# Optimization experiments

Hardware: AMD Instinct MI355X
Metric: run time of the kernel (lower is better)

The kernel has to match this reference:

```python
import jax, jax.numpy as jnp
import numpy as np

N_CLASSES = 10
NBD_PAD = 1
EPS = 1e-5  # nn.LayerNorm default eps


def _neighbor_states(state, n):
    # state: [B, n_classes, H, W]; replicates F.unfold(kernel=2n+1, padding=n)
    # then drops the center tap. Kernel positions enumerated row-major, matching
    # unfold's (C, K2) channel ordering after the view in the torch code.
    B, C, H, W = state.shape
    k = 2 * n + 1
    center = (k * k) // 2
    padded = jnp.pad(state, ((0, 0), (0, 0), (n, n), (n, n)))
    shifts = []
    for idx in range(k * k):
        if idx == center:
            continue
        ki, kj = divmod(idx, k)
        shifts.append(padded[:, :, ki:ki + H, kj:kj + W])
    nb = jnp.stack(shifts, axis=2)  # [B, C, K2-1, H, W]
    return nb.reshape(B, C * (k * k - 1), H, W)


def setup_inputs() -> dict:
    key = jax.random.key(0)
    ks = jax.random.split(key, 7)
    B, C, H, W = 64, 32, 128, 128
    NN_HID, PERC = 128, 112
    x = jax.random.normal(ks[0], (B, C, H, W), dtype=jnp.float32)
    w1 = jax.random.normal(ks[1], (NN_HID, PERC), dtype=jnp.float32) * (1.0 / np.sqrt(PERC))
    b1 = jax.random.normal(ks[2], (NN_HID,), dtype=jnp.float32) * 0.02
    w2 = jax.random.normal(ks[3], (C, NN_HID), dtype=jnp.float32) * (1.0 / np.sqrt(NN_HID))
    b2 = jax.random.normal(ks[4], (C,), dtype=jnp.float32) * 0.02
    gamma = jnp.ones((C,), dtype=jnp.float32) + 0.1 * jax.random.normal(ks[5], (C,), dtype=jnp.float32)
    beta = 0.1 * jax.random.normal(ks[6], (C,), dtype=jnp.float32)
    return {"x": x, "w1": w1, "b1": b1, "w2": w2, "b2": b2, "gamma": gamma, "beta": beta}


def reference(x, w1, b1, w2, b2, gamma, beta):
    # perceive: [B, in_ch + n_classes*(K2-1), H, W]
    nb = _neighbor_states(x[:, :N_CLASSES], NBD_PAD)
    perc = jnp.concatenate([x, nb], axis=1)
    # 1x1 conv MLP (fire_rate == 1.0 -> no update mask)
    h = jax.nn.relu(jnp.einsum('bchw,oc->bohw', perc, w1) + b1[None, :, None, None])
    dx = jnp.einsum('bchw,oc->bohw', h, w2) + b2[None, :, None, None]
    new_state = x + dx
    # clean_slate_if_white: zero hidden channels where argmax class == 0 (no_grad mask)
    pred = jnp.argmax(new_state[:, :N_CLASSES], axis=1)  # [B,H,W]
    inv = jax.lax.stop_gradient((pred != 0).astype(new_state.dtype))[:, None]  # [B,1,H,W]
    new_state = jnp.concatenate(
        [new_state[:, :N_CLASSES], new_state[:, N_CLASSES:] * inv], axis=1)
    # LayerNorm over channel dim (torch permutes to NHWC, norms last dim, permutes back)
    mu = jnp.mean(new_state, axis=1, keepdims=True)
    var = jnp.var(new_state, axis=1, keepdims=True)
    xn = (new_state - mu) * jax.lax.rsqrt(var + EPS)
    return xn * gamma[None, :, None, None] + beta[None, :, None, None]
```

## Files before the change

kernel.cpp:

```cpp
#include <hip/hip_runtime.h>

typedef unsigned short U16;
typedef unsigned int U32;
typedef __bf16 bf16;
typedef bf16 bf16x8 __attribute__((ext_vector_type(8)));
typedef U16  u16x8  __attribute__((ext_vector_type(8)));
typedef float f32x4 __attribute__((ext_vector_type(4)));

__device__ __forceinline__ void split3(float a, U16& o1, U16& o2, U16& o3) {
    U32 ua = __float_as_uint(a);
    float a1 = __uint_as_float(ua & 0xFFFF0000u);
    float r1 = a - a1;
    U32 u2 = __float_as_uint(r1);
    float a2 = __uint_as_float(u2 & 0xFFFF0000u);
    float r2 = r1 - a2;
    o1 = (U16)(ua >> 16);
    o2 = (U16)(u2 >> 16);
    o3 = (U16)(__float_as_uint(r2) >> 16);
}

__device__ __forceinline__ void split3x8(const float v[8], bf16x8& A1, bf16x8& A2, bf16x8& A3) {
    u16x8 e1, e2, e3;
    #pragma unroll
    for (int j = 0; j < 8; ++j) { U16 a, b, c; split3(v[j], a, b, c); e1[j] = a; e2[j] = b; e3[j] = c; }
    A1 = __builtin_bit_cast(bf16x8, e1);
    A2 = __builtin_bit_cast(bf16x8, e2);
    A3 = __builtin_bit_cast(bf16x8, e3);
}

__global__ __launch_bounds__(256)
void prep_kernel(const float* __restrict__ w1g, const float* __restrict__ w2g,
                 U16* __restrict__ w1L, U16* __restrict__ w2L)
{
    int tid = blockIdx.x * 256 + threadIdx.x;
    if (tid < 2048) {
        int n = tid >> 4, k0 = (tid & 15) << 3;
        float v[8];
        #pragma unroll
        for (int j = 0; j < 8; ++j) { int k = k0 + j; v[j] = (k < 112) ? w1g[n * 112 + k] : 0.0f; }
        bf16x8 L1, L2, L3; split3x8(v, L1, L2, L3);
        *(bf16x8*)(w1L + 0 * 16384 + n * 128 + k0) = L1;
        *(bf16x8*)(w1L + 1 * 16384 + n * 128 + k0) = L2;
        *(bf16x8*)(w1L + 2 * 16384 + n * 128 + k0) = L3;
    }
    if (tid < 512) {
        int n = tid >> 4, k0 = (tid & 15) << 3;
        float v[8];
        #pragma unroll
        for (int j = 0; j < 8; ++j) v[j] = w2g[n * 128 + k0 + j];
        bf16x8 L1, L2, L3; split3x8(v, L1, L2, L3);
        *(bf16x8*)(w2L + 0 * 4096 + n * 128 + k0) = L1;
        *(bf16x8*)(w2L + 1 * 4096 + n * 128 + k0) = L2;
        *(bf16x8*)(w2L + 2 * 4096 + n * 128 + k0) = L3;
    }
}

__global__ __launch_bounds__(256, 3)
void cann_kernel(const float* __restrict__ xg,  const U16* __restrict__ w1L,
                 const U16* __restrict__ w2L,
                 const float* __restrict__ b1g, const float* __restrict__ b2g,
                 const float* __restrict__ gg,  const float* __restrict__ bg,
                 float* __restrict__ outg)
{
    __shared__ __align__(16) U16 sL[3 * 8704];

    const int tid  = threadIdx.x;
    const int bid  = blockIdx.x;
    const int jseg = bid & 1;
    const int irow = (bid >> 1) & 127;
    const int b    = bid >> 8;
    const int jbase = jseg << 6;
    const int lane = tid & 63;
    const int wv   = tid >> 6;
    const int quad = lane >> 4;
    const int col  = lane & 15;

    {
        int px = tid & 63;
        int cg = tid >> 6;
        const float* src = xg + (b * 32 + cg * 8) * 16384 + irow * 128 + jbase + px;
        float v[8];
        #pragma unroll
        for (int i = 0; i < 8; ++i) v[i] = src[i * 16384];
        bf16x8 L1, L2, L3; split3x8(v, L1, L2, L3);
        int o = px * 136 + cg * 8;
        *(bf16x8*)&sL[o] = L1;
        *(bf16x8*)&sL[8704 + o] = L2;
        *(bf16x8*)&sL[17408 + o] = L3;

        #pragma unroll
        for (int pass = 0; pass < 3; ++pass) {
            int j = tid + pass * 256;
            if (j < 640) {
                int tpx = j & 63, cls = j >> 6;
                const float* cbase = xg + (b * 32 + cls) * 16384;
                float tv[8];
                #pragma unroll
                for (int t = 0; t < 8; ++t) {
                    int di = (int)((0x22211000u >> (4 * t)) & 0xFu) - 1;
                    int dj = (int)((0x21020210u >> (4 * t)) & 0xFu) - 1;
                    int row = irow + di;
                    int cc  = jbase + tpx + dj;
                    tv[t] = ((unsigned)row < 128u && (unsigned)cc < 128u)
                            ? cbase[row * 128 + cc] : 0.0f;
                }
                bf16x8 T1, T2, T3; split3x8(tv, T1, T2, T3);
                int to = tpx * 136 + 32 + cls * 8;
                *(bf16x8*)&sL[to] = T1;
                *(bf16x8*)&sL[8704 + to] = T2;
                *(bf16x8*)&sL[17408 + to] = T3;
            }
        }
        if (tid < 128) {
            int zo = (tid >> 1) * 136 + 112 + (tid & 1) * 8;
            uint4 z = make_uint4(0u, 0u, 0u, 0u);
            *(uint4*)&sL[zo] = z;
            *(uint4*)&sL[8704 + zo] = z;
            *(uint4*)&sL[17408 + zo] = z;
        }
    }

    bf16x8 bw1[3][2][4];
    #pragma unroll
    for (int n2 = 0; n2 < 2; ++n2)
        #pragma unroll
        for (int ks = 0; ks < 4; ++ks) {
            int n  = wv * 32 + n2 * 16 + col;
            int k0 = ks * 32 + quad * 8;
            #pragma unroll
            for (int L = 0; L < 3; ++L)
                bw1[L][n2][ks] = *(const bf16x8*)(w1L + L * 16384 + n * 128 + k0);
        }
    const float b1v0 = b1g[wv * 32 + col];
    const float b1v1 = b1g[wv * 32 + 16 + col];
    const float b2v0 = b2g[col];
    const float b2v1 = b2g[16 + col];

    float xs[2][4];
    #pragma unroll
    for (int n2 = 0; n2 < 2; ++n2)
        #pragma unroll
        for (int r = 0; r < 4; ++r)
            xs[n2][r] = xg[(b * 32 + n2 * 16 + col) * 16384 + irow * 128 + jbase
                           + wv * 16 + quad * 4 + r];

    __syncthreads();

    const f32x4 fz = {0.f, 0.f, 0.f, 0.f};
    f32x4 acc1[4][2];
    #pragma unroll
    for (int mt = 0; mt < 4; ++mt) { acc1[mt][0] = fz; acc1[mt][1] = fz; }

    #pragma unroll
    for (int mt = 0; mt < 4; ++mt) {
        #pragma unroll
        for (int ks = 0; ks < 4; ++ks) {
            int ao = (mt * 16 + col) * 136 + ks * 32 + quad * 8;
            bf16x8 A1 = *(const bf16x8*)&sL[ao];
            bf16x8 A2 = *(const bf16x8*)&sL[8704 + ao];
            bf16x8 A3 = *(const bf16x8*)&sL[17408 + ao];
            #pragma unroll
            for (int n2 = 0; n2 < 2; ++n2) {
                f32x4 a = acc1[mt][n2];
                a = __builtin_amdgcn_mfma_f32_16x16x32_bf16(A1, bw1[0][n2][ks], a, 0, 0, 0);
                a = __builtin_amdgcn_mfma_f32_16x16x32_bf16(A1, bw1[1][n2][ks], a, 0, 0, 0);
                a = __builtin_amdgcn_mfma_f32_16x16x32_bf16(A2, bw1[0][n2][ks], a, 0, 0, 0);
                a = __builtin_amdgcn_mfma_f32_16x16x32_bf16(A1, bw1[2][n2][ks], a, 0, 0, 0);
                a = __builtin_amdgcn_mfma_f32_16x16x32_bf16(A2, bw1[1][n2][ks], a, 0, 0, 0);
                a = __builtin_amdgcn_mfma_f32_16x16x32_bf16(A3, bw1[0][n2][ks], a, 0, 0, 0);
                acc1[mt][n2] = a;
            }
        }
    }
    __syncthreads();

    #pragma unroll
    for (int mt = 0; mt < 4; ++mt)
        #pragma unroll
        for (int n2 = 0; n2 < 2; ++n2) {
            float bb = n2 ? b1v1 : b1v0;
            #pragma unroll
            for (int r = 0; r < 4; ++r) {
                float v = fmaxf(acc1[mt][n2][r] + bb, 0.0f);
                U16 u1, u2, u3; split3(v, u1, u2, u3);
                int ho = (mt * 16 + quad * 4 + r) * 136 + wv * 32 + n2 * 16 + col;
                sL[ho] = u1; sL[8704 + ho] = u2; sL[17408 + ho] = u3;
            }
        }
    __syncthreads();

    f32x4 acc2[2];
    acc2[0] = fz; acc2[1] = fz;
    #pragma unroll
    for (int ks = 0; ks < 4; ++ks) {
        int k0 = ks * 32 + quad * 8;
        int ho = (wv * 16 + col) * 136 + k0;
        bf16x8 H1 = *(const bf16x8*)&sL[ho];
        bf16x8 H2 = *(const bf16x8*)&sL[8704 + ho];
        bf16x8 H3 = *(const bf16x8*)&sL[17408 + ho];
        #pragma unroll
        for (int n2 = 0; n2 < 2; ++n2) {
            int bo = (n2 * 16 + col) * 128 + k0;
            bf16x8 B1 = *(const bf16x8*)(w2L + 0 * 4096 + bo);
            bf16x8 B2 = *(const bf16x8*)(w2L + 1 * 4096 + bo);
            bf16x8 B3 = *(const bf16x8*)(w2L + 2 * 4096 + bo);
            f32x4 a = acc2[n2];
            a = __builtin_amdgcn_mfma_f32_16x16x32_bf16(H1, B1, a, 0, 0, 0);
            a = __builtin_amdgcn_mfma_f32_16x16x32_bf16(H1, B2, a, 0, 0, 0);
            a = __builtin_amdgcn_mfma_f32_16x16x32_bf16(H2, B1, a, 0, 0, 0);
            a = __builtin_amdgcn_mfma_f32_16x16x32_bf16(H1, B3, a, 0, 0, 0);
            a = __builtin_amdgcn_mfma_f32_16x16x32_bf16(H2, B2, a, 0, 0, 0);
            a = __builtin_amdgcn_mfma_f32_16x16x32_bf16(H3, B1, a, 0, 0, 0);
            acc2[n2] = a;
        }
    }
    __syncthreads();

    float* dxl = (float*)sL;
    #pragma unroll
    for (int n2 = 0; n2 < 2; ++n2) {
        float bb = n2 ? b2v1 : b2v0;
        int c = n2 * 16 + col;
        #pragma unroll
        for (int r = 0; r < 4; ++r) {
            int p = wv * 16 + quad * 4 + r;
            dxl[p * 33 + c] = acc2[n2][r] + bb + xs[n2][r];
        }
    }
    __syncthreads();

    if (tid < 64) {
        int p = tid;
        float ns[32];
        #pragma unroll
        for (int c = 0; c < 32; ++c) ns[c] = dxl[p * 33 + c];
        float m = ns[1];
        #pragma unroll
        for (int c = 2; c < 10; ++c) m = fmaxf(m, ns[c]);
        float keep = (m > ns[0]) ? 1.0f : 0.0f;
        #pragma unroll
        for (int c = 10; c < 32; ++c) ns[c] *= keep;
        float s = 0.f;
        #pragma unroll
        for (int c = 0; c < 32; ++c) s += ns[c];
        float mu = s * 0.03125f;
        float var = 0.f;
        #pragma unroll
        for (int c = 0; c < 32; ++c) { float d = ns[c] - mu; var += d * d; }
        var *= 0.03125f;
        float rstd = 1.0f / sqrtf(var + 1e-5f);
        int base = b * 524288 + irow * 128 + jbase + p;
        #pragma unroll
        for (int c = 0; c < 32; ++c)
            outg[base + c * 16384] = (ns[c] - mu) * rstd * gg[c] + bg[c];
    }
}

extern "C" void kernel_launch(void* const* d_in, const int* in_sizes, int n_in,
                              void* d_out, int out_size, void* d_ws, size_t ws_size,
                              hipStream_t stream) {
    const float* x  = (const float*)d_in[0];
    const float* w1 = (const float*)d_in[1];
    const float* b1 = (const float*)d_in[2];
    const float* w2 = (const float*)d_in[3];
    const float* b2 = (const float*)d_in[4];
    const float* g  = (const float*)d_in[5];
    const float* be = (const float*)d_in[6];
    float* out = (float*)d_out;

    U16* w1L = (U16*)d_ws;
    U16* w2L = (U16*)((char*)d_ws + 98304);

    hipLaunchKernelGGL(prep_kernel, dim3(8), dim3(256), 0, stream, w1, w2, w1L, w2L);
    hipLaunchKernelGGL(cann_kernel, dim3(16384), dim3(256), 0, stream,
                       x, w1L, w2L, b1, b2, g, be, out);
}
```

Baseline: 584.2 us.

## Prefetch inputs early, double-buffer weight fragments, and parallelize LayerNorm epilogue via shuffles

```diff
diff --git a/kernel.cpp b/kernel.cpp
--- a/kernel.cpp
+++ b/kernel.cpp
@@ -55,6 +55,34 @@
     }
 }
 
+__device__ __forceinline__ void tap_load(const float* __restrict__ xg, int b, int irow,
+                                         int jbase, int j, float v[8])
+{
+    int tpx = j & 63, cls = j >> 6;
+    const float* cbase = xg + (b * 32 + cls) * 16384;
+    #pragma unroll
+    for (int t = 0; t < 8; ++t) {
+        int di = (int)((0x22211000u >> (4 * t)) & 0xFu) - 1;
+        int dj = (int)((0x21020210u >> (4 * t)) & 0xFu) - 1;
+        int row = irow + di;
+        int cc  = jbase + tpx + dj;
+        bool okb = ((unsigned)row < 128u) && ((unsigned)cc < 128u);
+        int off = okb ? (row * 128 + cc) : 0;
+        float x = cbase[off];
+        v[t] = okb ? x : 0.0f;
+    }
+}
+
+__device__ __forceinline__ void tap_write(U16* sL, int j, const float v[8])
+{
+    int tpx = j & 63, cls = j >> 6;
+    bf16x8 T1, T2, T3; split3x8(v, T1, T2, T3);
+    int to = tpx * 136 + 32 + cls * 8;
+    *(bf16x8*)&sL[to] = T1;
+    *(bf16x8*)&sL[8704 + to] = T2;
+    *(bf16x8*)&sL[17408 + to] = T3;
+}
+
 __global__ __launch_bounds__(256, 3)
 void cann_kernel(const float* __restrict__ xg,  const U16* __restrict__ w1L,
                  const U16* __restrict__ w2L,
@@ -65,7 +93,8 @@
     __shared__ __align__(16) U16 sL[3 * 8704];
 
     const int tid  = threadIdx.x;
-    const int bid  = blockIdx.x;
+    const int bid0 = blockIdx.x;
+    const int bid  = (bid0 & 7) * 2048 + (bid0 >> 3);
     const int jseg = bid & 1;
     const int irow = (bid >> 1) & 127;
     const int b    = bid >> 8;
@@ -75,86 +104,80 @@
     const int quad = lane >> 4;
     const int col  = lane & 15;
 
+    const int px = tid & 63, cg = tid >> 6;
+    const float* srcA = xg + (b * 32 + cg * 8) * 16384 + irow * 128 + jbase + px;
+    float va[8];
+    #pragma unroll
+    for (int i = 0; i < 8; ++i) va[i] = srcA[i * 16384];
+
+    float vt0[8], vt1[8], vt2[8];
+    tap_load(xg, b, irow, jbase, tid,       vt0);
+    tap_load(xg, b, irow, jbase, tid + 256, vt1);
+    if (tid < 128) tap_load(xg, b, irow, jbase, tid + 512, vt2);
+
+    float xs[2][4];
+    #pragma unroll
+    for (int n2 = 0; n2 < 2; ++n2)
+        #pragma unroll
+        for (int r = 0; r < 4; ++r)
+            xs[n2][r] = xg[(b * 32 + n2 * 16 + col) * 16384 + irow * 128 + jbase
+                           + wv * 16 + quad * 4 + r];
+
+    const float b1v0 = b1g[wv * 32 + col];
+    const float b1v1 = b1g[wv * 32 + 16 + col];
+    const float b2v0 = b2g[col];
+    const float b2v1 = b2g[16 + col];
+    float g2v[2], be2v[2];
+    g2v[0] = gg[col];      g2v[1] = gg[16 + col];
+    be2v[0] = bg[col];     be2v[1] = bg[16 + col];
+
     {
-        int px = tid & 63;
-        int cg = tid >> 6;
-        const float* src = xg + (b * 32 + cg * 8) * 16384 + irow * 128 + jbase + px;
-        float v[8];
-        #pragma unroll
-        for (int i = 0; i < 8; ++i) v[i] = src[i * 16384];
-        bf16x8 L1, L2, L3; split3x8(v, L1, L2, L3);
+        bf16x8 L1, L2, L3; split3x8(va, L1, L2, L3);
         int o = px * 136 + cg * 8;
         *(bf16x8*)&sL[o] = L1;
         *(bf16x8*)&sL[8704 + o] = L2;
         *(bf16x8*)&sL[17408 + o] = L3;
-
-        #pragma unroll
-        for (int pass = 0; pass < 3; ++pass) {
-            int j = tid + pass * 256;
-            if (j < 640) {
-                int tpx = j & 63, cls = j >> 6;
-                const float* cbase = xg + (b * 32 + cls) * 16384;
-                float tv[8];
-                #pragma unroll
-                for (int t = 0; t < 8; ++t) {
-                    int di = (int)((0x22211000u >> (4 * t)) & 0xFu) - 1;
-                    int dj = (int)((0x21020210u >> (4 * t)) & 0xFu) - 1;
-                    int row = irow + di;
-                    int cc  = jbase + tpx + dj;
-                    tv[t] = ((unsigned)row < 128u && (unsigned)cc < 128u)
-                            ? cbase[row * 128 + cc] : 0.0f;
-                }
-                bf16x8 T1, T2, T3; split3x8(tv, T1, T2, T3);
-                int to = tpx * 136 + 32 + cls * 8;
-                *(bf16x8*)&sL[to] = T1;
-                *(bf16x8*)&sL[8704 + to] = T2;
-                *(bf16x8*)&sL[17408 + to] = T3;
-            }
-        }
-        if (tid < 128) {
-            int zo = (tid >> 1) * 136 + 112 + (tid & 1) * 8;
-            uint4 z = make_uint4(0u, 0u, 0u, 0u);
-            *(uint4*)&sL[zo] = z;
-            *(uint4*)&sL[8704 + zo] = z;
-            *(uint4*)&sL[17408 + zo] = z;
-        }
-    }
-
-    bf16x8 bw1[3][2][4];
-    #pragma unroll
-    for (int n2 = 0; n2 < 2; ++n2)
-        #pragma unroll
-        for (int ks = 0; ks < 4; ++ks) {
-            int n  = wv * 32 + n2 * 16 + col;
-            int k0 = ks * 32 + quad * 8;
+    }
+    tap_write(sL, tid,       vt0);
+    tap_write(sL, tid + 256, vt1);
+    if (tid < 128) tap_write(sL, tid + 512, vt2);
+    if (tid < 128) {
+        int zo = (tid >> 1) * 136 + 112 + (tid & 1) * 8;
+        uint4 z = make_uint4(0u, 0u, 0u, 0u);
+        *(uint4*)&sL[zo] = z;
+        *(uint4*)&sL[8704 + zo] = z;
+        *(uint4*)&sL[17408 + zo] = z;
+    }
+
+    const int n0r = wv * 32 + col;
+    bf16x8 bw[2][6];
+    #pragma unroll
+    for (int L = 0; L < 3; ++L)
+        #pragma unroll
+        for (int n2 = 0; n2 < 2; ++n2)
+            bw[0][L * 2 + n2] =
+                *(const bf16x8*)(w1L + L * 16384 + (n0r + n2 * 16) * 128 + quad * 8);
+
+    __syncthreads();
+
+    const f32x4 fz = {0.f, 0.f, 0.f, 0.f};
+    f32x4 acc1[4][2];
+    #pragma unroll
+    for (int mt = 0; mt < 4; ++mt) { acc1[mt][0] = fz; acc1[mt][1] = fz; }
+
+    #pragma unroll
+    for (int ks = 0; ks < 4; ++ks) {
+        if (ks < 3) {
             #pragma unroll
             for (int L = 0; L < 3; ++L)
-                bw1[L][n2][ks] = *(const bf16x8*)(w1L + L * 16384 + n * 128 + k0);
-        }
-    const float b1v0 = b1g[wv * 32 + col];
-    const float b1v1 = b1g[wv * 32 + 16 + col];
-    const float b2v0 = b2g[col];
-    const float b2v1 = b2g[16 + col];
-
-    float xs[2][4];
-    #pragma unroll
-    for (int n2 = 0; n2 < 2; ++n2)
-        #pragma unroll
-        for (int r = 0; r < 4; ++r)
-            xs[n2][r] = xg[(b * 32 + n2 * 16 + col) * 16384 + irow * 128 + jbase
-                           + wv * 16 + quad * 4 + r];
-
-    __syncthreads();
-
-    const f32x4 fz = {0.f, 0.f, 0.f, 0.f};
-    f32x4 acc1[4][2];
-    #pragma unroll
-    for (int mt = 0; mt < 4; ++mt) { acc1[mt][0] = fz; acc1[mt][1] = fz; }
-
-    #pragma unroll
-    for (int mt = 0; mt < 4; ++mt) {
-        #pragma unroll
-        for (int ks = 0; ks < 4; ++ks) {
+                #pragma unroll
+                for (int n2 = 0; n2 < 2; ++n2)
+                    bw[(ks + 1) & 1][L * 2 + n2] =
+                        *(const bf16x8*)(w1L + L * 16384 + (n0r + n2 * 16) * 128
+                                         + (ks + 1) * 32 + quad * 8);
+        }
+        #pragma unroll
+        for (int mt = 0; mt < 4; ++mt) {
             int ao = (mt * 16 + col) * 136 + ks * 32 + quad * 8;
             bf16x8 A1 = *(const bf16x8*)&sL[ao];
             bf16x8 A2 = *(const bf16x8*)&sL[8704 + ao];
@@ -162,12 +185,12 @@
             #pragma unroll
             for (int n2 = 0; n2 < 2; ++n2) {
                 f32x4 a = acc1[mt][n2];
-                a = __builtin_amdgcn_mfma_f32_16x16x32_bf16(A1, bw1[0][n2][ks], a, 0, 0, 0);
-                a = __builtin_amdgcn_mfma_f32_16x16x32_bf16(A1, bw1[1][n2][ks], a, 0, 0, 0);
-                a = __builtin_amdgcn_mfma_f32_16x16x32_bf16(A2, bw1[0][n2][ks], a, 0, 0, 0);
-                a = __builtin_amdgcn_mfma_f32_16x16x32_bf16(A1, bw1[2][n2][ks], a, 0, 0, 0);
-                a = __builtin_amdgcn_mfma_f32_16x16x32_bf16(A2, bw1[1][n2][ks], a, 0, 0, 0);
-                a = __builtin_amdgcn_mfma_f32_16x16x32_bf16(A3, bw1[0][n2][ks], a, 0, 0, 0);
+                a = __builtin_amdgcn_mfma_f32_16x16x32_bf16(A1, bw[ks & 1][0 + n2], a, 0, 0, 0);
+                a = __builtin_amdgcn_mfma_f32_16x16x32_bf16(A1, bw[ks & 1][2 + n2], a, 0, 0, 0);
+                a = __builtin_amdgcn_mfma_f32_16x16x32_bf16(A2, bw[ks & 1][0 + n2], a, 0, 0, 0);
+                a = __builtin_amdgcn_mfma_f32_16x16x32_bf16(A1, bw[ks & 1][4 + n2], a, 0, 0, 0);
+                a = __builtin_amdgcn_mfma_f32_16x16x32_bf16(A2, bw[ks & 1][2 + n2], a, 0, 0, 0);
+                a = __builtin_amdgcn_mfma_f32_16x16x32_bf16(A3, bw[ks & 1][0 + n2], a, 0, 0, 0);
                 acc1[mt][n2] = a;
             }
         }
@@ -187,72 +210,95 @@
                 sL[ho] = u1; sL[8704 + ho] = u2; sL[17408 + ho] = u3;
             }
         }
+
+    bf16x8 w2f[2][6];
+    #pragma unroll
+    for (int L = 0; L < 3; ++L)
+        #pragma unroll
+        for (int n2 = 0; n2 < 2; ++n2)
+            w2f[0][L * 2 + n2] =
+                *(const bf16x8*)(w2L + L * 4096 + (n2 * 16 + col) * 128 + quad * 8);
+
     __syncthreads();
 
     f32x4 acc2[2];
     acc2[0] = fz; acc2[1] = fz;
     #pragma unroll
     for (int ks = 0; ks < 4; ++ks) {
-        int k0 = ks * 32 + quad * 8;
-        int ho = (wv * 16 + col) * 136 + k0;
+        if (ks < 3) {
+            #pragma unroll
+            for (int L = 0; L < 3; ++L)
+                #pragma unroll
+                for (int n2 = 0; n2 < 2; ++n2)
+                    w2f[(ks + 1) & 1][L * 2 + n2] =
+                        *(const bf16x8*)(w2L + L * 4096 + (n2 * 16 + col) * 128
+                                         + (ks + 1) * 32 + quad * 8);
+        }
+        int ho = (wv * 16 + col) * 136 + ks * 32 + quad * 8;
         bf16x8 H1 = *(const bf16x8*)&sL[ho];
         bf16x8 H2 = *(const bf16x8*)&sL[8704 + ho];
         bf16x8 H3 = *(const bf16x8*)&sL[17408 + ho];
         #pragma unroll
         for (int n2 = 0; n2 < 2; ++n2) {
-            int bo = (n2 * 16 + col) * 128 + k0;
-            bf16x8 B1 = *(const bf16x8*)(w2L + 0 * 4096 + bo);
-            bf16x8 B2 = *(const bf16x8*)(w2L + 1 * 4096 + bo);
-            bf16x8 B3 = *(const bf16x8*)(w2L + 2 * 4096 + bo);
             f32x4 a = acc2[n2];
-            a = __builtin_amdgcn_mfma_f32_16x16x32_bf16(H1, B1, a, 0, 0, 0);
-            a = __builtin_amdgcn_mfma_f32_16x16x32_bf16(H1, B2, a, 0, 0, 0);
-            a = __builtin_amdgcn_mfma_f32_16x16x32_bf16(H2, B1, a, 0, 0, 0);
-            a = __builtin_amdgcn_mfma_f32_16x16x32_bf16(H1, B3, a, 0, 0, 0);
-            a = __builtin_amdgcn_mfma_f32_16x16x32_bf16(H2, B2, a, 0, 0, 0);
-            a = __builtin_amdgcn_mfma_f32_16x16x32_bf16(H3, B1, a, 0, 0, 0);
+            a = __builtin_amdgcn_mfma_f32_16x16x32_bf16(H1, w2f[ks & 1][0 + n2], a, 0, 0, 0);
+            a = __builtin_amdgcn_mfma_f32_16x16x32_bf16(H1, w2f[ks & 1][2 + n2], a, 0, 0, 0);
+            a = __builtin_amdgcn_mfma_f32_16x16x32_bf16(H2, w2f[ks & 1][0 + n2], a, 0, 0, 0);
+            a = __builtin_amdgcn_mfma_f32_16x16x32_bf16(H1, w2f[ks & 1][4 + n2], a, 0, 0, 0);
+            a = __builtin_amdgcn_mfma_f32_16x16x32_bf16(H2, w2f[ks & 1][2 + n2], a, 0, 0, 0);
+            a = __builtin_amdgcn_mfma_f32_16x16x32_bf16(H3, w2f[ks & 1][0 + n2], a, 0, 0, 0);
             acc2[n2] = a;
         }
     }
+
+    float fin[2][4];
+    #pragma unroll
+    for (int r = 0; r < 4; ++r) {
+        float n0 = acc2[0][r] + b2v0 + xs[0][r];
+        float n1 = acc2[1][r] + b2v1 + xs[1][r];
+        float cm = (col >= 1 && col <= 9) ? n0 : -3.0e38f;
+        float z0 = (col == 0)             ? n0 : -3.0e38f;
+        #pragma unroll
+        for (int m = 1; m < 16; m <<= 1) {
+            cm = fmaxf(cm, __shfl_xor(cm, m, 64));
+            z0 = fmaxf(z0, __shfl_xor(z0, m, 64));
+        }
+        float keep = (cm > z0) ? 1.0f : 0.0f;
+        n0 = (col >= 10) ? n0 * keep : n0;
+        n1 = n1 * keep;
+        float s = n0 + n1;
+        float q = n0 * n0 + n1 * n1;
+        #pragma unroll
+        for (int m = 1; m < 16; m <<= 1) {
+            s += __shfl_xor(s, m, 64);
+            q += __shfl_xor(q, m, 64);
+        }
+        float mu  = s * 0.03125f;
+        float var = q * 0.03125f - mu * mu;
+        float rstd = 1.0f / sqrtf(var + 1e-5f);
+        fin[0][r] = (n0 - mu) * rstd * g2v[0] + be2v[0];
+        fin[1][r] = (n1 - mu) * rstd * g2v[1] + be2v[1];
+    }
+
     __syncthreads();
 
     float* dxl = (float*)sL;
     #pragma unroll
-    for (int n2 = 0; n2 < 2; ++n2) {
-        float bb = n2 ? b2v1 : b2v0;
-        int c = n2 * 16 + col;
+    for (int n2 = 0; n2 < 2; ++n2)
         #pragma unroll
         for (int r = 0; r < 4; ++r) {
             int p = wv * 16 + quad * 4 + r;
-            dxl[p * 33 + c] = acc2[n2][r] + bb + xs[n2][r];
-        }
-    }
-    __syncthreads();
-
-    if (tid < 64) {
-        int p = tid;
-        float ns[32];
-        #pragma unroll
-        for (int c = 0; c < 32; ++c) ns[c] = dxl[p * 33 + c];
-        float m = ns[1];
-        #pragma unroll
-        for (int c = 2; c < 10; ++c) m = fmaxf(m, ns[c]);
-        float keep = (m > ns[0]) ? 1.0f : 0.0f;
-        #pragma unroll
-        for (int c = 10; c < 32; ++c) ns[c] *= keep;
-        float s = 0.f;
-        #pragma unroll
-        for (int c = 0; c < 32; ++c) s += ns[c];
-        float mu = s * 0.03125f;
-        float var = 0.f;
-        #pragma unroll
-        for (int c = 0; c < 32; ++c) { float d = ns[c] - mu; var += d * d; }
-        var *= 0.03125f;
-        float rstd = 1.0f / sqrtf(var + 1e-5f);
+            dxl[p * 37 + n2 * 16 + col] = fin[n2][r];
+        }
+    __syncthreads();
+
+    {
+        int p  = tid & 63;
+        int c0 = (tid >> 6) * 8;
         int base = b * 524288 + irow * 128 + jbase + p;
         #pragma unroll
-        for (int c = 0; c < 32; ++c)
-            outg[base + c * 16384] = (ns[c] - mu) * rstd * gg[c] + bg[c];
+        for (int i = 0; i < 8; ++i)
+            outg[base + (c0 + i) * 16384] = dxl[p * 37 + c0 + i];
     }
 }
 
```

Measured after the change: 610.8 us. 4.6% more time.

## Prefetch weight fragments per k-step, swizzle block order, use lightweight barriers

Applied to the files above, without the earlier changes.

```diff
diff --git a/kernel.cpp b/kernel.cpp
--- a/kernel.cpp
+++ b/kernel.cpp
@@ -55,6 +55,89 @@
     }
 }
 
+#define WBAR() do { asm volatile("s_waitcnt lgkmcnt(0)" ::: "memory"); \
+                    __builtin_amdgcn_s_barrier();                      \
+                    asm volatile("" ::: "memory"); } while (0)
+#define RBAR() do { asm volatile("" ::: "memory");                     \
+                    __builtin_amdgcn_s_barrier();                      \
+                    asm volatile("" ::: "memory"); } while (0)
+
+__device__ __forceinline__ void tap_load(const float* __restrict__ xg, int b, int irow,
+                                         int jbase, int j, float v[8])
+{
+    int tpx = j & 63, cls = j >> 6;
+    const float* cbase = xg + (b * 32 + cls) * 16384;
+    #pragma unroll
+    for (int t = 0; t < 8; ++t) {
+        int di = (int)((0x22211000u >> (4 * t)) & 0xFu) - 1;
+        int dj = (int)((0x21020210u >> (4 * t)) & 0xFu) - 1;
+        int row = irow + di;
+        int cc  = jbase + tpx + dj;
+        bool okb = ((unsigned)row < 128u) && ((unsigned)cc < 128u);
+        int off = okb ? (row * 128 + cc) : 0;
+        float x = cbase[off];
+        v[t] = okb ? x : 0.0f;
+    }
+}
+
+__device__ __forceinline__ void tap_write(U16* sL, int j, const float v[8])
+{
+    int tpx = j & 63, cls = j >> 6;
+    bf16x8 T1, T2, T3; split3x8(v, T1, T2, T3);
+    int to = tpx * 136 + 32 + cls * 8;
+    *(bf16x8*)&sL[to] = T1;
+    *(bf16x8*)&sL[8704 + to] = T2;
+    *(bf16x8*)&sL[17408 + to] = T3;
+}
+
+#define LDW1(g, ks_) do {                                                    \
+    _Pragma("unroll") for (int L_ = 0; L_ < 3; ++L_)                         \
+    _Pragma("unroll") for (int n_ = 0; n_ < 2; ++n_)                         \
+        g[L_ * 2 + n_] = *(const bf16x8*)(w1p + L_ * 16384 + n_ * 2048 + (ks_) * 32); \
+} while (0)
+
+#define MFMA1(ks_, g) do {                                                   \
+    _Pragma("unroll") for (int mt_ = 0; mt_ < 4; ++mt_) {                    \
+        const int ao_ = (mt_ * 16 + col) * 136 + (ks_) * 32 + quad * 8;      \
+        bf16x8 A1_ = *(const bf16x8*)&sL[ao_];                               \
+        bf16x8 A2_ = *(const bf16x8*)&sL[8704 + ao_];                        \
+        bf16x8 A3_ = *(const bf16x8*)&sL[17408 + ao_];                       \
+        _Pragma("unroll") for (int n_ = 0; n_ < 2; ++n_) {                   \
+            f32x4 a_ = acc1[mt_][n_];                                        \
+            a_ = __builtin_amdgcn_mfma_f32_16x16x32_bf16(A1_, g[0 + n_], a_, 0, 0, 0); \
+            a_ = __builtin_amdgcn_mfma_f32_16x16x32_bf16(A1_, g[2 + n_], a_, 0, 0, 0); \
+            a_ = __builtin_amdgcn_mfma_f32_16x16x32_bf16(A2_, g[0 + n_], a_, 0, 0, 0); \
+            a_ = __builtin_amdgcn_mfma_f32_16x16x32_bf16(A1_, g[4 + n_], a_, 0, 0, 0); \
+            a_ = __builtin_amdgcn_mfma_f32_16x16x32_bf16(A2_, g[2 + n_], a_, 0, 0, 0); \
+            a_ = __builtin_amdgcn_mfma_f32_16x16x32_bf16(A3_, g[0 + n_], a_, 0, 0, 0); \
+            acc1[mt_][n_] = a_;                                              \
+        }                                                                    \
+    }                                                                        \
+} while (0)
+
+#define LDW2(q, ks_) do {                                                    \
+    _Pragma("unroll") for (int L_ = 0; L_ < 3; ++L_)                         \
+    _Pragma("unroll") for (int n_ = 0; n_ < 2; ++n_)                         \
+        q[L_ * 2 + n_] = *(const bf16x8*)(w2p + L_ * 4096 + n_ * 2048 + (ks_) * 32); \
+} while (0)
+
+#define MFMA2(ks_, q) do {                                                   \
+    const int ho_ = (wv * 16 + col) * 136 + (ks_) * 32 + quad * 8;           \
+    bf16x8 H1_ = *(const bf16x8*)&sL[ho_];                                   \
+    bf16x8 H2_ = *(const bf16x8*)&sL[8704 + ho_];                            \
+    bf16x8 H3_ = *(const bf16x8*)&sL[17408 + ho_];                           \
+    _Pragma("unroll") for (int n_ = 0; n_ < 2; ++n_) {                       \
+        f32x4 a_ = acc2[n_];                                                 \
+        a_ = __builtin_amdgcn_mfma_f32_16x16x32_bf16(H1_, q[0 + n_], a_, 0, 0, 0); \
+        a_ = __builtin_amdgcn_mfma_f32_16x16x32_bf16(H1_, q[2 + n_], a_, 0, 0, 0); \
+        a_ = __builtin_amdgcn_mfma_f32_16x16x32_bf16(H2_, q[0 + n_], a_, 0, 0, 0); \
+        a_ = __builtin_amdgcn_mfma_f32_16x16x32_bf16(H1_, q[4 + n_], a_, 0, 0, 0); \
+        a_ = __builtin_amdgcn_mfma_f32_16x16x32_bf16(H2_, q[2 + n_], a_, 0, 0, 0); \
+        a_ = __builtin_amdgcn_mfma_f32_16x16x32_bf16(H3_, q[0 + n_], a_, 0, 0, 0); \
+        acc2[n_] = a_;                                                       \
+    }                                                                        \
+} while (0)
+
 __global__ __launch_bounds__(256, 3)
 void cann_kernel(const float* __restrict__ xg,  const U16* __restrict__ w1L,
                  const U16* __restrict__ w2L,
@@ -65,7 +148,8 @@
     __shared__ __align__(16) U16 sL[3 * 8704];
 
     const int tid  = threadIdx.x;
-    const int bid  = blockIdx.x;
+    const int bid0 = blockIdx.x;
+    const int bid  = (bid0 & 7) * 2048 + (bid0 >> 3);
     const int jseg = bid & 1;
     const int irow = (bid >> 1) & 127;
     const int b    = bid >> 8;
@@ -74,68 +158,42 @@
     const int wv   = tid >> 6;
     const int quad = lane >> 4;
     const int col  = lane & 15;
+    const int px   = tid & 63;
+    const int cg   = tid >> 6;
+
+    const U16* w1p = w1L + (wv * 32 + col) * 128 + quad * 8;
+    const U16* w2p = w2L + col * 128 + quad * 8;
 
     {
-        int px = tid & 63;
-        int cg = tid >> 6;
         const float* src = xg + (b * 32 + cg * 8) * 16384 + irow * 128 + jbase + px;
-        float v[8];
-        #pragma unroll
-        for (int i = 0; i < 8; ++i) v[i] = src[i * 16384];
-        bf16x8 L1, L2, L3; split3x8(v, L1, L2, L3);
+        float va[8];
+        #pragma unroll
+        for (int i = 0; i < 8; ++i) va[i] = src[i * 16384];
+        bf16x8 L1, L2, L3; split3x8(va, L1, L2, L3);
         int o = px * 136 + cg * 8;
         *(bf16x8*)&sL[o] = L1;
         *(bf16x8*)&sL[8704 + o] = L2;
         *(bf16x8*)&sL[17408 + o] = L3;
-
-        #pragma unroll
-        for (int pass = 0; pass < 3; ++pass) {
-            int j = tid + pass * 256;
-            if (j < 640) {
-                int tpx = j & 63, cls = j >> 6;
-                const float* cbase = xg + (b * 32 + cls) * 16384;
-                float tv[8];
-                #pragma unroll
-                for (int t = 0; t < 8; ++t) {
-                    int di = (int)((0x22211000u >> (4 * t)) & 0xFu) - 1;
-                    int dj = (int)((0x21020210u >> (4 * t)) & 0xFu) - 1;
-                    int row = irow + di;
-                    int cc  = jbase + tpx + dj;
-                    tv[t] = ((unsigned)row < 128u && (unsigned)cc < 128u)
-                            ? cbase[row * 128 + cc] : 0.0f;
-                }
-                bf16x8 T1, T2, T3; split3x8(tv, T1, T2, T3);
-                int to = tpx * 136 + 32 + cls * 8;
-                *(bf16x8*)&sL[to] = T1;
-                *(bf16x8*)&sL[8704 + to] = T2;
-                *(bf16x8*)&sL[17408 + to] = T3;
-            }
-        }
-        if (tid < 128) {
-            int zo = (tid >> 1) * 136 + 112 + (tid & 1) * 8;
-            uint4 z = make_uint4(0u, 0u, 0u, 0u);
-            *(uint4*)&sL[zo] = z;
-            *(uint4*)&sL[8704 + zo] = z;
-            *(uint4*)&sL[17408 + zo] = z;
-        }
-    }
-
-    bf16x8 bw1[3][2][4];
-    #pragma unroll
-    for (int n2 = 0; n2 < 2; ++n2)
-        #pragma unroll
-        for (int ks = 0; ks < 4; ++ks) {
-            int n  = wv * 32 + n2 * 16 + col;
-            int k0 = ks * 32 + quad * 8;
-            #pragma unroll
-            for (int L = 0; L < 3; ++L)
-                bw1[L][n2][ks] = *(const bf16x8*)(w1L + L * 16384 + n * 128 + k0);
-        }
+    }
+    {
+        float vt[8];
+        tap_load(xg, b, irow, jbase, tid, vt);       tap_write(sL, tid, vt);
+        tap_load(xg, b, irow, jbase, tid + 256, vt); tap_write(sL, tid + 256, vt);
+        if (tid < 128) { tap_load(xg, b, irow, jbase, tid + 512, vt);
+                         tap_write(sL, tid + 512, vt); }
+    }
+    if (tid < 128) {
+        int zo = (tid >> 1) * 136 + 112 + (tid & 1) * 8;
+        uint4 z = make_uint4(0u, 0u, 0u, 0u);
+        *(uint4*)&sL[zo] = z;
+        *(uint4*)&sL[8704 + zo] = z;
+        *(uint4*)&sL[17408 + zo] = z;
+    }
+
     const float b1v0 = b1g[wv * 32 + col];
     const float b1v1 = b1g[wv * 32 + 16 + col];
     const float b2v0 = b2g[col];
     const float b2v1 = b2g[16 + col];
-
     float xs[2][4];
     #pragma unroll
     for (int n2 = 0; n2 < 2; ++n2)
@@ -144,35 +202,32 @@
             xs[n2][r] = xg[(b * 32 + n2 * 16 + col) * 16384 + irow * 128 + jbase
                            + wv * 16 + quad * 4 + r];
 
-    __syncthreads();
+    bf16x8 g0[6], g1[6], g2[6], g3[6];
+    LDW1(g0, 0);
+    LDW1(g1, 1);
+
+    WBAR();
 
     const f32x4 fz = {0.f, 0.f, 0.f, 0.f};
     f32x4 acc1[4][2];
     #pragma unroll
     for (int mt = 0; mt < 4; ++mt) { acc1[mt][0] = fz; acc1[mt][1] = fz; }
 
-    #pragma unroll
-    for (int mt = 0; mt < 4; ++mt) {
-        #pragma unroll
-        for (int ks = 0; ks < 4; ++ks) {
-            int ao = (mt * 16 + col) * 136 + ks * 32 + quad * 8;
-            bf16x8 A1 = *(const bf16x8*)&sL[ao];
-            bf16x8 A2 = *(const bf16x8*)&sL[8704 + ao];
-            bf16x8 A3 = *(const bf16x8*)&sL[17408 + ao];
-            #pragma unroll
-            for (int n2 = 0; n2 < 2; ++n2) {
-                f32x4 a = acc1[mt][n2];
-                a = __builtin_amdgcn_mfma_f32_16x16x32_bf16(A1, bw1[0][n2][ks], a, 0, 0, 0);
-                a = __builtin_amdgcn_mfma_f32_16x16x32_bf16(A1, bw1[1][n2][ks], a, 0, 0, 0);
-                a = __builtin_amdgcn_mfma_f32_16x16x32_bf16(A2, bw1[0][n2][ks], a, 0, 0, 0);
-                a = __builtin_amdgcn_mfma_f32_16x16x32_bf16(A1, bw1[2][n2][ks], a, 0, 0, 0);
-                a = __builtin_amdgcn_mfma_f32_16x16x32_bf16(A2, bw1[1][n2][ks], a, 0, 0, 0);
-                a = __builtin_amdgcn_mfma_f32_16x16x32_bf16(A3, bw1[0][n2][ks], a, 0, 0, 0);
-                acc1[mt][n2] = a;
-            }
-        }
-    }
-    __syncthreads();
+    LDW1(g2, 2);
+    __builtin_amdgcn_sched_group_barrier(0x20, 6, 0);
+    MFMA1(0, g0);
+    LDW1(g3, 3);
+    __builtin_amdgcn_sched_group_barrier(0x20, 6, 0);
+    MFMA1(1, g1);
+    MFMA1(2, g2);
+    MFMA1(3, g3);
+
+    RBAR();
+
+    bf16x8 q0[6], q1[6], q2[6], q3[6];
+    LDW2(q0, 0);
+    LDW2(q1, 1);
+    __builtin_amdgcn_sched_group_barrier(0x20, 12, 0);
 
     #pragma unroll
     for (int mt = 0; mt < 4; ++mt)
@@ -187,34 +242,22 @@
                 sL[ho] = u1; sL[8704 + ho] = u2; sL[17408 + ho] = u3;
             }
         }
-    __syncthreads();
+
+    WBAR();
 
     f32x4 acc2[2];
     acc2[0] = fz; acc2[1] = fz;
-    #pragma unroll
-    for (int ks = 0; ks < 4; ++ks) {
-        int k0 = ks * 32 + quad * 8;
-        int ho = (wv * 16 + col) * 136 + k0;
-        bf16x8 H1 = *(const bf16x8*)&sL[ho];
-        bf16x8 H2 = *(const bf16x8*)&sL[8704 + ho];
-        bf16x8 H3 = *(const bf16x8*)&sL[17408 + ho];
-        #pragma unroll
-        for (int n2 = 0; n2 < 2; ++n2) {
-            int bo = (n2 * 16 + col) * 128 + k0;
-            bf16x8 B1 = *(const bf16x8*)(w2L + 0 * 4096 + bo);
-            bf16x8 B2 = *(const bf16x8*)(w2L + 1 * 4096 + bo);
-            bf16x8 B3 = *(const bf16x8*)(w2L + 2 * 4096 + bo);
-            f32x4 a = acc2[n2];
-            a = __builtin_amdgcn_mfma_f32_16x16x32_bf16(H1, B1, a, 0, 0, 0);
-            a = __builtin_amdgcn_mfma_f32_16x16x32_bf16(H1, B2, a, 0, 0, 0);
-            a = __builtin_amdgcn_mfma_f32_16x16x32_bf16(H2, B1, a, 0, 0, 0);
-            a = __builtin_amdgcn_mfma_f32_16x16x32_bf16(H1, B3, a, 0, 0, 0);
-            a = __builtin_amdgcn_mfma_f32_16x16x32_bf16(H2, B2, a, 0, 0, 0);
-            a = __builtin_amdgcn_mfma_f32_16x16x32_bf16(H3, B1, a, 0, 0, 0);
-            acc2[n2] = a;
-        }
-    }
-    __syncthreads();
+
+    LDW2(q2, 2);
+    __builtin_amdgcn_sched_group_barrier(0x20, 6, 0);
+    MFMA2(0, q0);
+    LDW2(q3, 3);
+    __builtin_amdgcn_sched_group_barrier(0x20, 6, 0);
+    MFMA2(1, q1);
+    MFMA2(2, q2);
+    MFMA2(3, q3);
+
+    RBAR();
 
     float* dxl = (float*)sL;
     #pragma unroll
@@ -227,7 +270,8 @@
             dxl[p * 33 + c] = acc2[n2][r] + bb + xs[n2][r];
         }
     }
-    __syncthreads();
+
+    WBAR();
 
     if (tid < 64) {
         int p = tid;
```

Result: no change. 578.0 us (-1.1%).
